# Performance work log

Hardware: AMD Instinct MI355X
Metric: run time of the kernel (lower is better)

## Reference

```python
import jax, jax.numpy as jnp
import numpy as np

N_VARS = 50000   # number of variables (graph nodes)
N_TX = 200000    # number of transforms in the bucket (edges)
D = 32           # per-variable slice size (layout.sizes[v])


def setup_inputs() -> dict:
    key = jax.random.key(0)
    k1, k2, k3, k4, k5 = jax.random.split(key, 5)
    theta = jax.random.normal(k1, (N_VARS * D,), dtype=jnp.float32)  # flat variable buffer
    # stacked_params of one TransformBucket: per-transform Linear(D, D)
    W = jax.random.normal(k2, (N_TX, D, D), dtype=jnp.float32) / np.sqrt(D)
    b = jax.random.normal(k3, (N_TX, D), dtype=jnp.float32)
    src_ids = jax.random.randint(k4, (N_TX,), 0, N_VARS)  # gather_indices rows (var id -> slice)
    tgt_ids = jax.random.randint(k5, (N_TX,), 0, N_VARS)  # scatter_indices rows
    return {"theta": theta, "W": W, "b": b, "src_ids": src_ids, "tgt_ids": tgt_ids}


def reference(theta, W, b, src_ids, tgt_ids):
    # Flat buffer viewed as [n_vars, D]; each variable slice is contiguous per Layout.
    tv = theta.reshape(N_VARS, D)
    # Bucketized gather: pull src slices for every transform in the bucket. [E, D]
    x = tv[src_ids]
    # vmapped transform application (stacked Linear params). [E, D]
    preds_e = jnp.einsum("eij,ej->ei", W, x) + b
    # Scatter-reduce predictions back into shared flat layout. [n_vars, D]
    preds = jnp.zeros_like(tv).at[tgt_ids].add(preds_e)
    # Energy residual per variable slice (gaussian energy: 0.5*||theta - pred||^2).
    resid = tv - preds
    return resid.reshape(-1)
```

## Files before the change

kernel.cpp:

```cpp
#include <hip/hip_runtime.h>

#define N_VARS 50000
#define N_TX   200000
#define DSZ    32

#define NWAVES 4000
#define NPAIRS (N_TX / 2)
#define PAIRS_PER_WAVE (NPAIRS / NWAVES)

typedef float f32x4 __attribute__((ext_vector_type(4)));

__global__ void copy_theta_kernel(const float4* __restrict__ theta,
                                  float4* __restrict__ out, int n4) {
    int i = blockIdx.x * blockDim.x + threadIdx.x;
    int stride = gridDim.x * blockDim.x;
    for (; i < n4; i += stride) out[i] = theta[i];
}

__global__ __launch_bounds__(256)
void transform_scatter_kernel(const float* __restrict__ theta,
                              const float* __restrict__ W,
                              const float* __restrict__ bia,
                              const int* __restrict__ src,
                              const int* __restrict__ tgt,
                              float* __restrict__ out) {
    const int lane = threadIdx.x & 63;
    const int wave = (blockIdx.x * blockDim.x + threadIdx.x) >> 6;

    const int j0     = (lane & 7) << 2;
    const int g      = lane >> 3;
    const int myRow  = (lane & 3) * 8 + g;
    const bool hiB   = (lane & 4) != 0;

    int p  = wave;
    int sA = src[2 * p], sB = src[2 * p + 1];
    int tA = tgt[2 * p], tB = tgt[2 * p + 1];

    #pragma unroll 1
    for (int it = 0; it < PAIRS_PER_WAVE; ++it) {
        const int e = 2 * p;

        const f32x4 xA = *reinterpret_cast<const f32x4*>(theta + (size_t)sA * DSZ + j0);
        const f32x4 xB = *reinterpret_cast<const f32x4*>(theta + (size_t)sB * DSZ + j0);

        const f32x4* WA = reinterpret_cast<const f32x4*>(W + (size_t)e * (DSZ * DSZ));
        const f32x4* WB = WA + 256;

        const f32x4 a0 = __builtin_nontemporal_load(WA +   0 + lane);
        const f32x4 a1 = __builtin_nontemporal_load(WA +  64 + lane);
        const f32x4 a2 = __builtin_nontemporal_load(WA + 128 + lane);
        const f32x4 a3 = __builtin_nontemporal_load(WA + 192 + lane);
        const f32x4 c0 = __builtin_nontemporal_load(WB +   0 + lane);
        const f32x4 c1 = __builtin_nontemporal_load(WB +  64 + lane);
        const f32x4 c2 = __builtin_nontemporal_load(WB + 128 + lane);
        const f32x4 c3 = __builtin_nontemporal_load(WB + 192 + lane);

        const float biasv =
            __builtin_nontemporal_load(bia + ((size_t)e + (hiB ? 1 : 0)) * DSZ + myRow);

        const int pn = p + NWAVES;
        const int pc = (it + 1 < PAIRS_PER_WAVE) ? pn : wave;
        const int sA2 = src[2 * pc], sB2 = src[2 * pc + 1];
        const int tA2 = tgt[2 * pc], tB2 = tgt[2 * pc + 1];

        float pA0 = a0.x * xA.x + a0.y * xA.y + a0.z * xA.z + a0.w * xA.w;
        float pA1 = a1.x * xA.x + a1.y * xA.y + a1.z * xA.z + a1.w * xA.w;
        float pA2 = a2.x * xA.x + a2.y * xA.y + a2.z * xA.z + a2.w * xA.w;
        float pA3 = a3.x * xA.x + a3.y * xA.y + a3.z * xA.z + a3.w * xA.w;
        float pB0 = c0.x * xB.x + c0.y * xB.y + c0.z * xB.z + c0.w * xB.w;
        float pB1 = c1.x * xB.x + c1.y * xB.y + c1.z * xB.z + c1.w * xB.w;
        float pB2 = c2.x * xB.x + c2.y * xB.y + c2.z * xB.z + c2.w * xB.w;
        float pB3 = c3.x * xB.x + c3.y * xB.y + c3.z * xB.z + c3.w * xB.w;

        #pragma unroll
        for (int m = 1; m <= 4; m <<= 1) {
            pA0 += __shfl_xor(pA0, m); pA1 += __shfl_xor(pA1, m);
            pA2 += __shfl_xor(pA2, m); pA3 += __shfl_xor(pA3, m);
            pB0 += __shfl_xor(pB0, m); pB1 += __shfl_xor(pB1, m);
            pB2 += __shfl_xor(pB2, m); pB3 += __shfl_xor(pB3, m);
        }

        const int   r   = lane & 3;
        const float sA_ = (r == 0) ? pA0 : (r == 1) ? pA1 : (r == 2) ? pA2 : pA3;
        const float sB_ = (r == 0) ? pB0 : (r == 1) ? pB1 : (r == 2) ? pB2 : pB3;
        const float val = hiB ? sB_ : sA_;
        const int   te  = hiB ? tB : tA;

        atomicAdd(out + (size_t)te * DSZ + myRow, -(val + biasv));

        p = pn; sA = sA2; sB = sB2; tA = tA2; tB = tB2;
    }
}

extern "C" void kernel_launch(void* const* d_in, const int* in_sizes, int n_in,
                              void* d_out, int out_size, void* d_ws, size_t ws_size,
                              hipStream_t stream) {
    const float* theta = (const float*)d_in[0];
    const float* W     = (const float*)d_in[1];
    const float* b     = (const float*)d_in[2];
    const int*   src   = (const int*)d_in[3];
    const int*   tgt   = (const int*)d_in[4];
    float* out = (float*)d_out;

    const int n4 = (N_VARS * DSZ) / 4;
    copy_theta_kernel<<<1024, 256, 0, stream>>>((const float4*)theta, (float4*)out, n4);

    transform_scatter_kernel<<<NWAVES / 4, 256, 0, stream>>>(theta, W, b, src, tgt, out);
}
```

Baseline: 155.5 us.

## Use a butterfly shuffle reduction, plain loads, and a one-element-per-thread copy

Replaces the 24-shuffle full reduction with a recursive-halving butterfly that needs only 7 shuffles. Replaces the nontemporal W/bias loads with ordinary loads and drops the software prefetch of the next src/tgt indices in favour of int2 loads inside the loop. Changes the theta copy kernel from a grid-stride loop to one element per thread with a full grid. Together these aim to cut shuffle and ALU work and launch-shape overhead, at the cost of losing the index prefetch and the cache-bypass hints on the streamed weights.

```diff
diff --git a/kernel.cpp b/kernel.cpp
--- a/kernel.cpp
+++ b/kernel.cpp
@@ -13,8 +13,7 @@
 __global__ void copy_theta_kernel(const float4* __restrict__ theta,
                                   float4* __restrict__ out, int n4) {
     int i = blockIdx.x * blockDim.x + threadIdx.x;
-    int stride = gridDim.x * blockDim.x;
-    for (; i < n4; i += stride) out[i] = theta[i];
+    if (i < n4) out[i] = theta[i];
 }
 
 __global__ __launch_bounds__(256)
@@ -27,41 +26,34 @@
     const int lane = threadIdx.x & 63;
     const int wave = (blockIdx.x * blockDim.x + threadIdx.x) >> 6;
 
-    const int j0     = (lane & 7) << 2;
-    const int g      = lane >> 3;
-    const int myRow  = (lane & 3) * 8 + g;
-    const bool hiB   = (lane & 4) != 0;
+    const int j0    = (lane & 7) << 2;
+    const int g     = lane >> 3;
+    const int myRow = (lane & 3) * 8 + g;
+    const int hiB   = (lane >> 2) & 1;
 
-    int p  = wave;
-    int sA = src[2 * p], sB = src[2 * p + 1];
-    int tA = tgt[2 * p], tB = tgt[2 * p + 1];
-
-    #pragma unroll 1
     for (int it = 0; it < PAIRS_PER_WAVE; ++it) {
+        const int p = wave + it * NWAVES;
         const int e = 2 * p;
 
-        const f32x4 xA = *reinterpret_cast<const f32x4*>(theta + (size_t)sA * DSZ + j0);
-        const f32x4 xB = *reinterpret_cast<const f32x4*>(theta + (size_t)sB * DSZ + j0);
+        const int2 sp = *reinterpret_cast<const int2*>(src + e);
+        const int2 tp = *reinterpret_cast<const int2*>(tgt + e);
+
+        const f32x4 xA = *reinterpret_cast<const f32x4*>(theta + (size_t)sp.x * DSZ + j0);
+        const f32x4 xB = *reinterpret_cast<const f32x4*>(theta + (size_t)sp.y * DSZ + j0);
 
         const f32x4* WA = reinterpret_cast<const f32x4*>(W + (size_t)e * (DSZ * DSZ));
         const f32x4* WB = WA + 256;
 
-        const f32x4 a0 = __builtin_nontemporal_load(WA +   0 + lane);
-        const f32x4 a1 = __builtin_nontemporal_load(WA +  64 + lane);
-        const f32x4 a2 = __builtin_nontemporal_load(WA + 128 + lane);
-        const f32x4 a3 = __builtin_nontemporal_load(WA + 192 + lane);
-        const f32x4 c0 = __builtin_nontemporal_load(WB +   0 + lane);
-        const f32x4 c1 = __builtin_nontemporal_load(WB +  64 + lane);
-        const f32x4 c2 = __builtin_nontemporal_load(WB + 128 + lane);
-        const f32x4 c3 = __builtin_nontemporal_load(WB + 192 + lane);
+        const f32x4 a0 = WA[  0 + lane];
+        const f32x4 a1 = WA[ 64 + lane];
+        const f32x4 a2 = WA[128 + lane];
+        const f32x4 a3 = WA[192 + lane];
+        const f32x4 c0 = WB[  0 + lane];
+        const f32x4 c1 = WB[ 64 + lane];
+        const f32x4 c2 = WB[128 + lane];
+        const f32x4 c3 = WB[192 + lane];
 
-        const float biasv =
-            __builtin_nontemporal_load(bia + ((size_t)e + (hiB ? 1 : 0)) * DSZ + myRow);
-
-        const int pn = p + NWAVES;
-        const int pc = (it + 1 < PAIRS_PER_WAVE) ? pn : wave;
-        const int sA2 = src[2 * pc], sB2 = src[2 * pc + 1];
-        const int tA2 = tgt[2 * pc], tB2 = tgt[2 * pc + 1];
+        const float biasv = bia[((size_t)e + hiB) * DSZ + myRow];
 
         float pA0 = a0.x * xA.x + a0.y * xA.y + a0.z * xA.z + a0.w * xA.w;
         float pA1 = a1.x * xA.x + a1.y * xA.y + a1.z * xA.z + a1.w * xA.w;
@@ -72,23 +64,29 @@
         float pB2 = c2.x * xB.x + c2.y * xB.y + c2.z * xB.z + c2.w * xB.w;
         float pB3 = c3.x * xB.x + c3.y * xB.y + c3.z * xB.z + c3.w * xB.w;
 
-        #pragma unroll
-        for (int m = 1; m <= 4; m <<= 1) {
-            pA0 += __shfl_xor(pA0, m); pA1 += __shfl_xor(pA1, m);
-            pA2 += __shfl_xor(pA2, m); pA3 += __shfl_xor(pA3, m);
-            pB0 += __shfl_xor(pB0, m); pB1 += __shfl_xor(pB1, m);
-            pB2 += __shfl_xor(pB2, m); pB3 += __shfl_xor(pB3, m);
-        }
+        const bool b0 = (lane & 1) != 0;
+        const bool b1 = (lane & 2) != 0;
+        const bool b2 = (lane & 4) != 0;
 
-        const int   r   = lane & 3;
-        const float sA_ = (r == 0) ? pA0 : (r == 1) ? pA1 : (r == 2) ? pA2 : pA3;
-        const float sB_ = (r == 0) ? pB0 : (r == 1) ? pB1 : (r == 2) ? pB2 : pB3;
-        const float val = hiB ? sB_ : sA_;
-        const int   te  = hiB ? tB : tA;
+        float vA01 = b0 ? pA1 : pA0, oA01 = b0 ? pA0 : pA1;
+        float vA23 = b0 ? pA3 : pA2, oA23 = b0 ? pA2 : pA3;
+        float vB01 = b0 ? pB1 : pB0, oB01 = b0 ? pB0 : pB1;
+        float vB23 = b0 ? pB3 : pB2, oB23 = b0 ? pB2 : pB3;
+        vA01 += __shfl_xor(oA01, 1);
+        vA23 += __shfl_xor(oA23, 1);
+        vB01 += __shfl_xor(oB01, 1);
+        vB23 += __shfl_xor(oB23, 1);
 
-        atomicAdd(out + (size_t)te * DSZ + myRow, -(val + biasv));
+        float vA = b1 ? vA23 : vA01, oA = b1 ? vA01 : vA23;
+        float vB = b1 ? vB23 : vB01, oB = b1 ? vB01 : vB23;
+        vA += __shfl_xor(oA, 2);
+        vB += __shfl_xor(oB, 2);
 
-        p = pn; sA = sA2; sB = sB2; tA = tA2; tB = tB2;
+        float v = b2 ? vB : vA, o = b2 ? vA : vB;
+        v += __shfl_xor(o, 4);
+
+        const int te = b2 ? tp.y : tp.x;
+        atomicAdd(out + (size_t)te * DSZ + myRow, -(v + biasv));
     }
 }
 
@@ -103,7 +101,8 @@
     float* out = (float*)d_out;
 
     const int n4 = (N_VARS * DSZ) / 4;
-    copy_theta_kernel<<<1024, 256, 0, stream>>>((const float4*)theta, (float4*)out, n4);
+    copy_theta_kernel<<<(n4 + 255) / 256, 256, 0, stream>>>(
+        (const float4*)theta, (float4*)out, n4);
 
     transform_scatter_kernel<<<NWAVES / 4, 256, 0, stream>>>(theta, W, b, src, tgt, out);
 }
```

Result: slower. 173.1 us (+11.3%).
